# Kernel tuning notes

Measured on AMD Instinct MI355X. Metric: run time of the kernel, lower is better.

The kernel has to match this reference:

```python
import jax, jax.numpy as jnp
import numpy as np

N = 50000   # nodes
E = 600000  # directed edges (avg degree ~12)
F_IN = 128
HID = 128
N_LAYERS = 7


def setup_inputs() -> dict:
    key = jax.random.key(0)
    ks = jax.random.split(key, 5)
    x = jax.random.normal(ks[0], (N, F_IN), dtype=jnp.float32)
    edge_index = jax.random.randint(ks[1], (2, E), 0, N, dtype=jnp.int64)
    Ws = jax.random.normal(ks[2], (N_LAYERS, F_IN, HID), dtype=jnp.float32) * 0.05
    bs = jnp.zeros((N_LAYERS, HID), dtype=jnp.float32)
    lin_w = jax.random.normal(ks[3], (HID, 1), dtype=jnp.float32) * 0.05
    lin_b = jnp.zeros((1,), dtype=jnp.float32)
    return {"x": x, "edge_index": edge_index, "Ws": Ws, "bs": bs,
            "lin_w": lin_w, "lin_b": lin_b}


def reference(x, edge_index, Ws, bs, lin_w, lin_b):
    n = x.shape[0]
    loop = jnp.arange(n, dtype=edge_index.dtype)
    # PyG GCNConv default: add self-loops, symmetric normalization.
    src = jnp.concatenate([edge_index[0], loop])  # [E+N] message sources (j)
    dst = jnp.concatenate([edge_index[1], loop])  # [E+N] message targets (i)
    deg = jax.ops.segment_sum(jnp.ones_like(dst, dtype=x.dtype), dst, num_segments=n)
    dis = jnp.where(deg > 0, jax.lax.rsqrt(deg), 0.0)  # deg^-1/2, 0 for isolated
    norm = dis[src] * dis[dst]                          # [E+N]

    def gcn_layer(h, W, b):
        h = h @ W                                        # linear first (as in PyG)
        msg = h[src] * norm[:, None]                     # gather + scale
        return jax.ops.segment_sum(msg, dst, num_segments=n) + b

    h = x
    for i in range(N_LAYERS):
        h = jax.nn.relu(gcn_layer(h, Ws[i], bs[i]))
    out = h @ lin_w + lin_b                              # [N, 1]
    return out.squeeze()                                 # [N]
```

## Files before the change

### kernel.cpp

```cpp
#include <hip/hip_runtime.h>

#define HID 128
#define ASPITCH 132
#define BM 64


__global__ __launch_bounds__(256) void k_count(const int* __restrict__ ei, int E,
                                               int* __restrict__ deg) {
    int e = blockIdx.x * 256 + threadIdx.x;
    if (e < E) atomicAdd(&deg[ei[E + e]], 1);
}

__global__ __launch_bounds__(256) void k_scan1(const int* __restrict__ deg,
                                               int* __restrict__ rowptr,
                                               int* __restrict__ partial, int n) {
    __shared__ int s[256];
    int tid = threadIdx.x;
    int i = blockIdx.x * 256 + tid;
    int v = (i < n) ? deg[i] : 0;
    s[tid] = v;
    __syncthreads();
    for (int off = 1; off < 256; off <<= 1) {
        int t = (tid >= off) ? s[tid - off] : 0;
        __syncthreads();
        s[tid] += t;
        __syncthreads();
    }
    if (i < n) rowptr[i] = s[tid] - v;
    if (tid == 255) partial[blockIdx.x] = s[255];
}

__global__ __launch_bounds__(256) void k_scan2(int* __restrict__ partial, int nb) {
    __shared__ int s[256];
    int tid = threadIdx.x;
    int v = (tid < nb) ? partial[tid] : 0;
    s[tid] = v;
    __syncthreads();
    for (int off = 1; off < 256; off <<= 1) {
        int t = (tid >= off) ? s[tid - off] : 0;
        __syncthreads();
        s[tid] += t;
        __syncthreads();
    }
    if (tid < nb) partial[tid] = s[tid] - v;
}

__global__ __launch_bounds__(256) void k_scan3(int* __restrict__ rowptr,
                                               const int* __restrict__ partial,
                                               int n, int E) {
    int i = blockIdx.x * 256 + threadIdx.x;
    if (i < n) rowptr[i] += partial[blockIdx.x];
    if (i == 0) rowptr[n] = E;
}

__global__ __launch_bounds__(256) void k_dis(const int* __restrict__ deg,
                                             float* __restrict__ dis, int n) {
    int i = blockIdx.x * 256 + threadIdx.x;
    if (i < n) dis[i] = 1.0f / sqrtf((float)(deg[i] + 1));
}

__global__ __launch_bounds__(256) void k_fill(const int* __restrict__ ei, int E,
                                              const int* __restrict__ rowptr,
                                              int* __restrict__ cursor,
                                              int* __restrict__ col) {
    int e = blockIdx.x * 256 + threadIdx.x;
    if (e < E) {
        int d = ei[E + e];
        int p = atomicAdd(&cursor[d], 1);
        col[rowptr[d] + p] = ei[e];
    }
}


__global__ __launch_bounds__(256, 3) void k_gemm(const float* __restrict__ A,
                                                 const float* __restrict__ W,
                                                 const float* __restrict__ dis,
                                                 float* __restrict__ T, int n) {
    __shared__ float As[BM * ASPITCH];
    int r0 = blockIdx.x * BM;
    int tid = threadIdx.x;
    int rows = n - r0; if (rows > BM) rows = BM;
    {
        const float4* A4 = (const float4*)(A + (size_t)r0 * HID);
        int tot = rows * (HID / 4);
        for (int i = tid; i < tot; i += 256) {
            int row = i >> 5, c = (i & 31) << 2;
            *(float4*)&As[row * ASPITCH + c] = A4[i];
        }
    }
    __syncthreads();

    int tx = tid & 31, ty = tid >> 5;
    int rr0 = ty * 8;
    const float4* W4 = (const float4*)W;

    float acc[8][4];
    #pragma unroll
    for (int r = 0; r < 8; ++r) { acc[r][0]=0.f; acc[r][1]=0.f; acc[r][2]=0.f; acc[r][3]=0.f; }

    float4 wa0 = W4[0 * 32 + tx];
    float4 wa1 = W4[1 * 32 + tx];
    float4 wa2 = W4[2 * 32 + tx];
    float4 wa3 = W4[3 * 32 + tx];
    float4 wb0, wb1, wb2, wb3;

    #pragma unroll 1
    for (int k = 0; k < HID; k += 8) {
        wb0 = W4[(k + 4) * 32 + tx];
        wb1 = W4[(k + 5) * 32 + tx];
        wb2 = W4[(k + 6) * 32 + tx];
        wb3 = W4[(k + 7) * 32 + tx];
        #pragma unroll
        for (int r = 0; r < 8; ++r) {
            float4 a = *(const float4*)&As[(rr0 + r) * ASPITCH + k];
            acc[r][0] = fmaf(a.x, wa0.x, acc[r][0]);
            acc[r][1] = fmaf(a.x, wa0.y, acc[r][1]);
            acc[r][2] = fmaf(a.x, wa0.z, acc[r][2]);
            acc[r][3] = fmaf(a.x, wa0.w, acc[r][3]);
            acc[r][0] = fmaf(a.y, wa1.x, acc[r][0]);
            acc[r][1] = fmaf(a.y, wa1.y, acc[r][1]);
            acc[r][2] = fmaf(a.y, wa1.z, acc[r][2]);
            acc[r][3] = fmaf(a.y, wa1.w, acc[r][3]);
            acc[r][0] = fmaf(a.z, wa2.x, acc[r][0]);
            acc[r][1] = fmaf(a.z, wa2.y, acc[r][1]);
            acc[r][2] = fmaf(a.z, wa2.z, acc[r][2]);
            acc[r][3] = fmaf(a.z, wa2.w, acc[r][3]);
            acc[r][0] = fmaf(a.w, wa3.x, acc[r][0]);
            acc[r][1] = fmaf(a.w, wa3.y, acc[r][1]);
            acc[r][2] = fmaf(a.w, wa3.z, acc[r][2]);
            acc[r][3] = fmaf(a.w, wa3.w, acc[r][3]);
        }
        if (k + 8 < HID) {
            wa0 = W4[(k + 8)  * 32 + tx];
            wa1 = W4[(k + 9)  * 32 + tx];
            wa2 = W4[(k + 10) * 32 + tx];
            wa3 = W4[(k + 11) * 32 + tx];
        }
        #pragma unroll
        for (int r = 0; r < 8; ++r) {
            float4 a = *(const float4*)&As[(rr0 + r) * ASPITCH + k + 4];
            acc[r][0] = fmaf(a.x, wb0.x, acc[r][0]);
            acc[r][1] = fmaf(a.x, wb0.y, acc[r][1]);
            acc[r][2] = fmaf(a.x, wb0.z, acc[r][2]);
            acc[r][3] = fmaf(a.x, wb0.w, acc[r][3]);
            acc[r][0] = fmaf(a.y, wb1.x, acc[r][0]);
            acc[r][1] = fmaf(a.y, wb1.y, acc[r][1]);
            acc[r][2] = fmaf(a.y, wb1.z, acc[r][2]);
            acc[r][3] = fmaf(a.y, wb1.w, acc[r][3]);
            acc[r][0] = fmaf(a.z, wb2.x, acc[r][0]);
            acc[r][1] = fmaf(a.z, wb2.y, acc[r][1]);
            acc[r][2] = fmaf(a.z, wb2.z, acc[r][2]);
            acc[r][3] = fmaf(a.z, wb2.w, acc[r][3]);
            acc[r][0] = fmaf(a.w, wb3.x, acc[r][0]);
            acc[r][1] = fmaf(a.w, wb3.y, acc[r][1]);
            acc[r][2] = fmaf(a.w, wb3.z, acc[r][2]);
            acc[r][3] = fmaf(a.w, wb3.w, acc[r][3]);
        }
    }

    int c0 = tx * 4;
    #pragma unroll
    for (int r = 0; r < 8; ++r) {
        int row = rr0 + r;
        if (row < rows) {
            float d = dis[r0 + row];
            float4 o = make_float4(acc[r][0] * d, acc[r][1] * d, acc[r][2] * d, acc[r][3] * d);
            *(float4*)&T[(size_t)(r0 + row) * HID + c0] = o;
        }
    }
}

__global__ __launch_bounds__(256) void k_agg(const float* __restrict__ T,
                                             const int* __restrict__ rowptr,
                                             const int* __restrict__ col,
                                             const float* __restrict__ dis,
                                             const float* __restrict__ b,
                                             float* __restrict__ H, int n) {
    int node = (blockIdx.x * 256 + threadIdx.x) >> 5;
    int lane = threadIdx.x & 31;
    if (node >= n) return;
    size_t foff = (size_t)(lane * 4);
    size_t base = (size_t)node * HID + foff;
    float4 acc = *(const float4*)&T[base];
    float4 acc2 = make_float4(0.f, 0.f, 0.f, 0.f);
    int e = rowptr[node], e1 = rowptr[node + 1];
    for (; e + 8 <= e1; e += 8) {
        int j0 = col[e + 0];
        int j1 = col[e + 1];
        int j2 = col[e + 2];
        int j3 = col[e + 3];
        int j4 = col[e + 4];
        int j5 = col[e + 5];
        int j6 = col[e + 6];
        int j7 = col[e + 7];
        float4 v0 = *(const float4*)&T[(size_t)j0 * HID + foff];
        float4 v1 = *(const float4*)&T[(size_t)j1 * HID + foff];
        float4 v2 = *(const float4*)&T[(size_t)j2 * HID + foff];
        float4 v3 = *(const float4*)&T[(size_t)j3 * HID + foff];
        float4 v4 = *(const float4*)&T[(size_t)j4 * HID + foff];
        float4 v5 = *(const float4*)&T[(size_t)j5 * HID + foff];
        float4 v6 = *(const float4*)&T[(size_t)j6 * HID + foff];
        float4 v7 = *(const float4*)&T[(size_t)j7 * HID + foff];
        acc.x  += (v0.x + v1.x) + (v2.x + v3.x);
        acc.y  += (v0.y + v1.y) + (v2.y + v3.y);
        acc.z  += (v0.z + v1.z) + (v2.z + v3.z);
        acc.w  += (v0.w + v1.w) + (v2.w + v3.w);
        acc2.x += (v4.x + v5.x) + (v6.x + v7.x);
        acc2.y += (v4.y + v5.y) + (v6.y + v7.y);
        acc2.z += (v4.z + v5.z) + (v6.z + v7.z);
        acc2.w += (v4.w + v5.w) + (v6.w + v7.w);
    }
    for (; e + 2 <= e1; e += 2) {
        int j0 = col[e + 0];
        int j1 = col[e + 1];
        float4 v0 = *(const float4*)&T[(size_t)j0 * HID + foff];
        float4 v1 = *(const float4*)&T[(size_t)j1 * HID + foff];
        acc.x  += v0.x; acc.y  += v0.y; acc.z  += v0.z; acc.w  += v0.w;
        acc2.x += v1.x; acc2.y += v1.y; acc2.z += v1.z; acc2.w += v1.w;
    }
    if (e < e1) {
        int j = col[e];
        float4 v = *(const float4*)&T[(size_t)j * HID + foff];
        acc.x += v.x; acc.y += v.y; acc.z += v.z; acc.w += v.w;
    }
    acc.x += acc2.x; acc.y += acc2.y; acc.z += acc2.z; acc.w += acc2.w;
    float d = dis[node];
    float4 bb = *(const float4*)&b[lane * 4];
    float4 o;
    o.x = fmaxf(fmaf(d, acc.x, bb.x), 0.0f);
    o.y = fmaxf(fmaf(d, acc.y, bb.y), 0.0f);
    o.z = fmaxf(fmaf(d, acc.z, bb.z), 0.0f);
    o.w = fmaxf(fmaf(d, acc.w, bb.w), 0.0f);
    *(float4*)&H[base] = o;
}

__global__ __launch_bounds__(256) void k_final(const float* __restrict__ H,
                                               const float* __restrict__ w,
                                               const float* __restrict__ lb,
                                               float* __restrict__ out, int n) {
    int node = (blockIdx.x * 256 + threadIdx.x) >> 5;
    int lane = threadIdx.x & 31;
    if (node >= n) return;
    float4 h = *(const float4*)&H[(size_t)node * HID + lane * 4];
    float4 ww = *(const float4*)&w[lane * 4];
    float s = h.x * ww.x + h.y * ww.y + h.z * ww.z + h.w * ww.w;
    #pragma unroll
    for (int o = 16; o > 0; o >>= 1) s += __shfl_down(s, o, 64);
    if (lane == 0) out[node] = s + lb[0];
}


extern "C" void kernel_launch(void* const* d_in, const int* in_sizes, int n_in,
                              void* d_out, int out_size, void* d_ws, size_t ws_size,
                              hipStream_t stream) {
    const float* x     = (const float*)d_in[0];
    const int*   ei    = (const int*)d_in[1];
    const float* Ws    = (const float*)d_in[2];
    const float* bs    = (const float*)d_in[3];
    const float* lin_w = (const float*)d_in[4];
    const float* lin_b = (const float*)d_in[5];
    float* out = (float*)d_out;

    int n = in_sizes[0] / HID;
    int E = in_sizes[1] / 2;
    int L = in_sizes[2] / (HID * HID);

    char* ws = (char*)d_ws;
    size_t off = 0;
    auto alloc = [&](size_t bytes) -> void* {
        void* p = ws + off;
        off += (bytes + 255) & ~(size_t)255;
        return p;
    };
    int*   deg     = (int*)alloc((size_t)n * 4);
    int*   cursor  = (int*)alloc((size_t)n * 4);
    int*   rowptr  = (int*)alloc((size_t)(n + 1) * 4);
    int*   partial = (int*)alloc(1024);
    float* dis     = (float*)alloc((size_t)n * 4);
    int*   col     = (int*)alloc((size_t)E * 4);
    float* hbuf    = (float*)alloc((size_t)n * HID * 4);
    float* tbuf    = (float*)alloc((size_t)n * HID * 4);
    (void)ws_size;

    hipMemsetAsync(deg, 0, (size_t)n * 4, stream);
    hipMemsetAsync(cursor, 0, (size_t)n * 4, stream);

    int eb = (E + 255) / 256;
    int nb = (n + 255) / 256;
    k_count<<<eb, 256, 0, stream>>>(ei, E, deg);
    k_scan1<<<nb, 256, 0, stream>>>(deg, rowptr, partial, n);
    k_scan2<<<1, 256, 0, stream>>>(partial, nb);
    k_scan3<<<nb, 256, 0, stream>>>(rowptr, partial, n, E);
    k_dis<<<nb, 256, 0, stream>>>(deg, dis, n);
    k_fill<<<eb, 256, 0, stream>>>(ei, E, rowptr, cursor, col);

    const float* hin = x;
    int gb = (n + BM - 1) / BM;
    int hb = (n + 7) / 8;
    for (int l = 0; l < L; ++l) {
        k_gemm<<<gb, 256, 0, stream>>>(hin, Ws + (size_t)l * HID * HID, dis, tbuf, n);
        k_agg<<<hb, 256, 0, stream>>>(tbuf, rowptr, col, dis, bs + (size_t)l * HID, hbuf, n);
        hin = hbuf;
    }
    k_final<<<hb, 256, 0, stream>>>(hbuf, lin_w, lin_b, out, n);
}
```

Before: 622.4 us.

## Fuse neighbor aggregation with next layer GEMM and final linear projection

Aggregation of each layer (gather-sum, scale, bias, ReLU) is now done inside the next layer's GEMM kernel, staging the aggregated rows in shared memory instead of writing them to global memory. The last aggregation is fused with the output linear projection, removing the separate final kernel. This removes a full hidden-state write and read per layer plus several launches, at the cost of serializing 8 rows of gathering per warp-half within each block and using a larger unpadded shared tile, which reduces memory-level parallelism for the irregular gather.

```diff
diff --git a/kernel.cpp b/kernel.cpp
--- a/kernel.cpp
+++ b/kernel.cpp
@@ -72,10 +72,10 @@
 }
 
 
-__global__ __launch_bounds__(256, 3) void k_gemm(const float* __restrict__ A,
-                                                 const float* __restrict__ W,
-                                                 const float* __restrict__ dis,
-                                                 float* __restrict__ T, int n) {
+__global__ __launch_bounds__(256, 3) void k_gemm0(const float* __restrict__ A,
+                                                  const float* __restrict__ W,
+                                                  const float* __restrict__ dis,
+                                                  float* __restrict__ T, int n) {
     __shared__ float As[BM * ASPITCH];
     int r0 = blockIdx.x * BM;
     int tid = threadIdx.x;
@@ -170,18 +170,171 @@
     }
 }
 
-__global__ __launch_bounds__(256) void k_agg(const float* __restrict__ T,
-                                             const int* __restrict__ rowptr,
-                                             const int* __restrict__ col,
-                                             const float* __restrict__ dis,
-                                             const float* __restrict__ b,
-                                             float* __restrict__ H, int n) {
+__global__ __launch_bounds__(256, 3) void k_aggemm(const float* __restrict__ Uin,
+                                                   const float* __restrict__ W,
+                                                   const float* __restrict__ b,
+                                                   const float* __restrict__ dis,
+                                                   const int* __restrict__ rowptr,
+                                                   const int* __restrict__ col,
+                                                   float* __restrict__ Uout, int n) {
+    __shared__ float S[BM * HID];
+    int r0 = blockIdx.x * BM;
+    int tid = threadIdx.x;
+    int hw = tid >> 5, lane = tid & 31;
+    size_t foff = (size_t)(lane * 4);
+    float4 bb = *(const float4*)&b[lane * 4];
+
+    #pragma unroll 1
+    for (int rr = 0; rr < 8; ++rr) {
+        int row = r0 + hw * 8 + rr;
+        float4 acc = make_float4(0.f, 0.f, 0.f, 0.f);
+        if (row < n) {
+            acc = *(const float4*)&Uin[(size_t)row * HID + foff];
+            float4 acc2 = make_float4(0.f, 0.f, 0.f, 0.f);
+            int e = rowptr[row], e1 = rowptr[row + 1];
+            for (; e + 8 <= e1; e += 8) {
+                int j0 = col[e + 0];
+                int j1 = col[e + 1];
+                int j2 = col[e + 2];
+                int j3 = col[e + 3];
+                int j4 = col[e + 4];
+                int j5 = col[e + 5];
+                int j6 = col[e + 6];
+                int j7 = col[e + 7];
+                float4 v0 = *(const float4*)&Uin[(size_t)j0 * HID + foff];
+                float4 v1 = *(const float4*)&Uin[(size_t)j1 * HID + foff];
+                float4 v2 = *(const float4*)&Uin[(size_t)j2 * HID + foff];
+                float4 v3 = *(const float4*)&Uin[(size_t)j3 * HID + foff];
+                float4 v4 = *(const float4*)&Uin[(size_t)j4 * HID + foff];
+                float4 v5 = *(const float4*)&Uin[(size_t)j5 * HID + foff];
+                float4 v6 = *(const float4*)&Uin[(size_t)j6 * HID + foff];
+                float4 v7 = *(const float4*)&Uin[(size_t)j7 * HID + foff];
+                acc.x  += (v0.x + v1.x) + (v2.x + v3.x);
+                acc.y  += (v0.y + v1.y) + (v2.y + v3.y);
+                acc.z  += (v0.z + v1.z) + (v2.z + v3.z);
+                acc.w  += (v0.w + v1.w) + (v2.w + v3.w);
+                acc2.x += (v4.x + v5.x) + (v6.x + v7.x);
+                acc2.y += (v4.y + v5.y) + (v6.y + v7.y);
+                acc2.z += (v4.z + v5.z) + (v6.z + v7.z);
+                acc2.w += (v4.w + v5.w) + (v6.w + v7.w);
+            }
+            for (; e + 2 <= e1; e += 2) {
+                int j0 = col[e + 0];
+                int j1 = col[e + 1];
+                float4 v0 = *(const float4*)&Uin[(size_t)j0 * HID + foff];
+                float4 v1 = *(const float4*)&Uin[(size_t)j1 * HID + foff];
+                acc.x  += v0.x; acc.y  += v0.y; acc.z  += v0.z; acc.w  += v0.w;
+                acc2.x += v1.x; acc2.y += v1.y; acc2.z += v1.z; acc2.w += v1.w;
+            }
+            if (e < e1) {
+                int j = col[e];
+                float4 v = *(const float4*)&Uin[(size_t)j * HID + foff];
+                acc.x += v.x; acc.y += v.y; acc.z += v.z; acc.w += v.w;
+            }
+            float d = dis[row];
+            acc.x = fmaxf(fmaf(d, acc.x + acc2.x, bb.x), 0.0f);
+            acc.y = fmaxf(fmaf(d, acc.y + acc2.y, bb.y), 0.0f);
+            acc.z = fmaxf(fmaf(d, acc.z + acc2.z, bb.z), 0.0f);
+            acc.w = fmaxf(fmaf(d, acc.w + acc2.w, bb.w), 0.0f);
+        }
+        *(float4*)&S[(hw * 8 + rr) * HID + lane * 4] = acc;
+    }
+    __syncthreads();
+
+    int tx = tid & 31, ty = tid >> 5;
+    int rr0 = ty * 8;
+    const float4* W4 = (const float4*)W;
+
+    float acc[8][4];
+    #pragma unroll
+    for (int r = 0; r < 8; ++r) { acc[r][0]=0.f; acc[r][1]=0.f; acc[r][2]=0.f; acc[r][3]=0.f; }
+
+    float4 wa0 = W4[0 * 32 + tx];
+    float4 wa1 = W4[1 * 32 + tx];
+    float4 wa2 = W4[2 * 32 + tx];
+    float4 wa3 = W4[3 * 32 + tx];
+    float4 wb0, wb1, wb2, wb3;
+
+    #pragma unroll 1
+    for (int k = 0; k < HID; k += 8) {
+        wb0 = W4[(k + 4) * 32 + tx];
+        wb1 = W4[(k + 5) * 32 + tx];
+        wb2 = W4[(k + 6) * 32 + tx];
+        wb3 = W4[(k + 7) * 32 + tx];
+        #pragma unroll
+        for (int r = 0; r < 8; ++r) {
+            float4 a = *(const float4*)&S[(rr0 + r) * HID + k];
+            acc[r][0] = fmaf(a.x, wa0.x, acc[r][0]);
+            acc[r][1] = fmaf(a.x, wa0.y, acc[r][1]);
+            acc[r][2] = fmaf(a.x, wa0.z, acc[r][2]);
+            acc[r][3] = fmaf(a.x, wa0.w, acc[r][3]);
+            acc[r][0] = fmaf(a.y, wa1.x, acc[r][0]);
+            acc[r][1] = fmaf(a.y, wa1.y, acc[r][1]);
+            acc[r][2] = fmaf(a.y, wa1.z, acc[r][2]);
+            acc[r][3] = fmaf(a.y, wa1.w, acc[r][3]);
+            acc[r][0] = fmaf(a.z, wa2.x, acc[r][0]);
+            acc[r][1] = fmaf(a.z, wa2.y, acc[r][1]);
+            acc[r][2] = fmaf(a.z, wa2.z, acc[r][2]);
+            acc[r][3] = fmaf(a.z, wa2.w, acc[r][3]);
+            acc[r][0] = fmaf(a.w, wa3.x, acc[r][0]);
+            acc[r][1] = fmaf(a.w, wa3.y, acc[r][1]);
+            acc[r][2] = fmaf(a.w, wa3.z, acc[r][2]);
+            acc[r][3] = fmaf(a.w, wa3.w, acc[r][3]);
+        }
+        if (k + 8 < HID) {
+            wa0 = W4[(k + 8)  * 32 + tx];
+            wa1 = W4[(k + 9)  * 32 + tx];
+            wa2 = W4[(k + 10) * 32 + tx];
+            wa3 = W4[(k + 11) * 32 + tx];
+        }
+        #pragma unroll
+        for (int r = 0; r < 8; ++r) {
+            float4 a = *(const float4*)&S[(rr0 + r) * HID + k + 4];
+            acc[r][0] = fmaf(a.x, wb0.x, acc[r][0]);
+            acc[r][1] = fmaf(a.x, wb0.y, acc[r][1]);
+            acc[r][2] = fmaf(a.x, wb0.z, acc[r][2]);
+            acc[r][3] = fmaf(a.x, wb0.w, acc[r][3]);
+            acc[r][0] = fmaf(a.y, wb1.x, acc[r][0]);
+            acc[r][1] = fmaf(a.y, wb1.y, acc[r][1]);
+            acc[r][2] = fmaf(a.y, wb1.z, acc[r][2]);
+            acc[r][3] = fmaf(a.y, wb1.w, acc[r][3]);
+            acc[r][0] = fmaf(a.z, wb2.x, acc[r][0]);
+            acc[r][1] = fmaf(a.z, wb2.y, acc[r][1]);
+            acc[r][2] = fmaf(a.z, wb2.z, acc[r][2]);
+            acc[r][3] = fmaf(a.z, wb2.w, acc[r][3]);
+            acc[r][0] = fmaf(a.w, wb3.x, acc[r][0]);
+            acc[r][1] = fmaf(a.w, wb3.y, acc[r][1]);
+            acc[r][2] = fmaf(a.w, wb3.z, acc[r][2]);
+            acc[r][3] = fmaf(a.w, wb3.w, acc[r][3]);
+        }
+    }
+
+    int rows = n - r0; if (rows > BM) rows = BM;
+    int c0 = tx * 4;
+    #pragma unroll
+    for (int r = 0; r < 8; ++r) {
+        int row = rr0 + r;
+        if (row < rows) {
+            float d = dis[r0 + row];
+            float4 o = make_float4(acc[r][0] * d, acc[r][1] * d, acc[r][2] * d, acc[r][3] * d);
+            *(float4*)&Uout[(size_t)(r0 + row) * HID + c0] = o;
+        }
+    }
+}
+
+__global__ __launch_bounds__(256) void k_agglin(const float* __restrict__ Uin,
+                                                const float* __restrict__ b,
+                                                const float* __restrict__ dis,
+                                                const int* __restrict__ rowptr,
+                                                const int* __restrict__ col,
+                                                const float* __restrict__ lw,
+                                                const float* __restrict__ lb,
+                                                float* __restrict__ out, int n) {
     int node = (blockIdx.x * 256 + threadIdx.x) >> 5;
     int lane = threadIdx.x & 31;
     if (node >= n) return;
     size_t foff = (size_t)(lane * 4);
-    size_t base = (size_t)node * HID + foff;
-    float4 acc = *(const float4*)&T[base];
+    float4 acc = *(const float4*)&Uin[(size_t)node * HID + foff];
     float4 acc2 = make_float4(0.f, 0.f, 0.f, 0.f);
     int e = rowptr[node], e1 = rowptr[node + 1];
     for (; e + 8 <= e1; e += 8) {
@@ -193,14 +346,14 @@
         int j5 = col[e + 5];
         int j6 = col[e + 6];
         int j7 = col[e + 7];
-        float4 v0 = *(const float4*)&T[(size_t)j0 * HID + foff];
-        float4 v1 = *(const float4*)&T[(size_t)j1 * HID + foff];
-        float4 v2 = *(const float4*)&T[(size_t)j2 * HID + foff];
-        float4 v3 = *(const float4*)&T[(size_t)j3 * HID + foff];
-        float4 v4 = *(const float4*)&T[(size_t)j4 * HID + foff];
-        float4 v5 = *(const float4*)&T[(size_t)j5 * HID + foff];
-        float4 v6 = *(const float4*)&T[(size_t)j6 * HID + foff];
-        float4 v7 = *(const float4*)&T[(size_t)j7 * HID + foff];
+        float4 v0 = *(const float4*)&Uin[(size_t)j0 * HID + foff];
+        float4 v1 = *(const float4*)&Uin[(size_t)j1 * HID + foff];
+        float4 v2 = *(const float4*)&Uin[(size_t)j2 * HID + foff];
+        float4 v3 = *(const float4*)&Uin[(size_t)j3 * HID + foff];
+        float4 v4 = *(const float4*)&Uin[(size_t)j4 * HID + foff];
+        float4 v5 = *(const float4*)&Uin[(size_t)j5 * HID + foff];
+        float4 v6 = *(const float4*)&Uin[(size_t)j6 * HID + foff];
+        float4 v7 = *(const float4*)&Uin[(size_t)j7 * HID + foff];
         acc.x  += (v0.x + v1.x) + (v2.x + v3.x);
         acc.y  += (v0.y + v1.y) + (v2.y + v3.y);
         acc.z  += (v0.z + v1.z) + (v2.z + v3.z);
@@ -213,36 +366,24 @@
     for (; e + 2 <= e1; e += 2) {
         int j0 = col[e + 0];
         int j1 = col[e + 1];
-        float4 v0 = *(const float4*)&T[(size_t)j0 * HID + foff];
-        float4 v1 = *(const float4*)&T[(size_t)j1 * HID + foff];
+        float4 v0 = *(const float4*)&Uin[(size_t)j0 * HID + foff];
+        float4 v1 = *(const float4*)&Uin[(size_t)j1 * HID + foff];
         acc.x  += v0.x; acc.y  += v0.y; acc.z  += v0.z; acc.w  += v0.w;
         acc2.x += v1.x; acc2.y += v1.y; acc2.z += v1.z; acc2.w += v1.w;
     }
     if (e < e1) {
         int j = col[e];
-        float4 v = *(const float4*)&T[(size_t)j * HID + foff];
+        float4 v = *(const float4*)&Uin[(size_t)j * HID + foff];
         acc.x += v.x; acc.y += v.y; acc.z += v.z; acc.w += v.w;
     }
-    acc.x += acc2.x; acc.y += acc2.y; acc.z += acc2.z; acc.w += acc2.w;
     float d = dis[node];
     float4 bb = *(const float4*)&b[lane * 4];
-    float4 o;
-    o.x = fmaxf(fmaf(d, acc.x, bb.x), 0.0f);
-    o.y = fmaxf(fmaf(d, acc.y, bb.y), 0.0f);
-    o.z = fmaxf(fmaf(d, acc.z, bb.z), 0.0f);
-    o.w = fmaxf(fmaf(d, acc.w, bb.w), 0.0f);
-    *(float4*)&H[base] = o;
-}
-
-__global__ __launch_bounds__(256) void k_final(const float* __restrict__ H,
-                                               const float* __restrict__ w,
-                                               const float* __restrict__ lb,
-                                               float* __restrict__ out, int n) {
-    int node = (blockIdx.x * 256 + threadIdx.x) >> 5;
-    int lane = threadIdx.x & 31;
-    if (node >= n) return;
-    float4 h = *(const float4*)&H[(size_t)node * HID + lane * 4];
-    float4 ww = *(const float4*)&w[lane * 4];
+    float4 h;
+    h.x = fmaxf(fmaf(d, acc.x + acc2.x, bb.x), 0.0f);
+    h.y = fmaxf(fmaf(d, acc.y + acc2.y, bb.y), 0.0f);
+    h.z = fmaxf(fmaf(d, acc.z + acc2.z, bb.z), 0.0f);
+    h.w = fmaxf(fmaf(d, acc.w + acc2.w, bb.w), 0.0f);
+    float4 ww = *(const float4*)&lw[lane * 4];
     float s = h.x * ww.x + h.y * ww.y + h.z * ww.z + h.w * ww.w;
     #pragma unroll
     for (int o = 16; o > 0; o >>= 1) s += __shfl_down(s, o, 64);
@@ -278,8 +419,8 @@
     int*   partial = (int*)alloc(1024);
     float* dis     = (float*)alloc((size_t)n * 4);
     int*   col     = (int*)alloc((size_t)E * 4);
-    float* hbuf    = (float*)alloc((size_t)n * HID * 4);
-    float* tbuf    = (float*)alloc((size_t)n * HID * 4);
+    float* ubuf0   = (float*)alloc((size_t)n * HID * 4);
+    float* ubuf1   = (float*)alloc((size_t)n * HID * 4);
     (void)ws_size;
 
     hipMemsetAsync(deg, 0, (size_t)n * 4, stream);
@@ -294,13 +435,20 @@
     k_dis<<<nb, 256, 0, stream>>>(deg, dis, n);
     k_fill<<<eb, 256, 0, stream>>>(ei, E, rowptr, cursor, col);
 
-    const float* hin = x;
     int gb = (n + BM - 1) / BM;
     int hb = (n + 7) / 8;
-    for (int l = 0; l < L; ++l) {
-        k_gemm<<<gb, 256, 0, stream>>>(hin, Ws + (size_t)l * HID * HID, dis, tbuf, n);
-        k_agg<<<hb, 256, 0, stream>>>(tbuf, rowptr, col, dis, bs + (size_t)l * HID, hbuf, n);
-        hin = hbuf;
-    }
-    k_final<<<hb, 256, 0, stream>>>(hbuf, lin_w, lin_b, out, n);
-}
+
+    k_gemm0<<<gb, 256, 0, stream>>>(x, Ws, dis, ubuf0, n);
+
+    float* uin = ubuf0;
+    float* uout = ubuf1;
+    for (int i = 0; i + 1 < L; ++i) {
+        k_aggemm<<<gb, 256, 0, stream>>>(uin, Ws + (size_t)(i + 1) * HID * HID,
+                                         bs + (size_t)i * HID, dis, rowptr, col,
+                                         uout, n);
+        float* t = uin; uin = uout; uout = t;
+    }
+
+    k_agglin<<<hb, 256, 0, stream>>>(uin, bs + (size_t)(L - 1) * HID, dis,
+                                     rowptr, col, lin_w, lin_b, out, n);
+}
```

Measured after the change: 568.3 us. -8.7%, faster.
